# Performance work log

Hardware: AMD Instinct MI355X
Metric: run time of the kernel (lower is better)

Reference implementation:

```python
import jax, jax.numpy as jnp
import numpy as np

B, S, DIM, H, DH = 2, 2048, 1024, 16, 64
EPS = 1e-6


def rms_norm(x, w):
    # x: (..., DH); computed in fp32 like the torch module
    norm = jax.lax.rsqrt(jnp.mean(jnp.square(x), axis=-1, keepdims=True) + EPS)
    return (x * norm) * w


def apply_rope(x, freqs):
    # x: (B, H, S, D), freqs: (S, D); torch code slices cos/sin to first half
    d = x.shape[-1] // 2
    cos = jnp.cos(freqs)[None, None, :, :d]
    sin = jnp.sin(freqs)[None, None, :, :d]
    x1, x2 = x[..., :d], x[..., d:]
    return jnp.concatenate([x1 * cos - x2 * sin, x2 * cos + x1 * sin], axis=-1)


def setup_inputs() -> dict:
    key = jax.random.key(0)
    ks = jax.random.split(key, 4)
    x = jax.random.normal(ks[0], (B, S, DIM), dtype=jnp.float32)
    # causal additive mask
    causal = jnp.tril(jnp.ones((S, S), dtype=bool))
    mask = jnp.where(causal, 0.0, -1e9).astype(jnp.float32)[None, None]
    # standard rope frequencies: pos * inv_freq over head_dim
    inv_freq = 1.0 / (10000.0 ** (jnp.arange(0, DH, dtype=jnp.float32) / DH))
    rope_freqs = jnp.arange(S, dtype=jnp.float32)[:, None] * inv_freq[None, :]
    total = H * DH
    w_qkv = jax.random.normal(ks[1], (3 * total, DIM), dtype=jnp.float32) * (DIM ** -0.5)
    w_out = jax.random.normal(ks[2], (DIM, total), dtype=jnp.float32) * (total ** -0.5)
    q_norm_w = jnp.ones((DH,), dtype=jnp.float32)
    k_norm_w = jnp.ones((DH,), dtype=jnp.float32)
    return {"x": x, "mask": mask, "rope_freqs": rope_freqs, "w_qkv": w_qkv,
            "w_out": w_out, "q_norm_w": q_norm_w, "k_norm_w": k_norm_w}


def reference(x, mask, rope_freqs, w_qkv, w_out, q_norm_w, k_norm_w):
    b, s, _ = x.shape
    qkv = (x @ w_qkv.T).reshape(b, s, 3, H, DH)
    q, k, v = qkv[:, :, 0], qkv[:, :, 1], qkv[:, :, 2]
    q = jnp.transpose(rms_norm(q, q_norm_w), (0, 2, 1, 3))  # (B,H,S,DH)
    k = jnp.transpose(rms_norm(k, k_norm_w), (0, 2, 1, 3))
    v = jnp.transpose(v, (0, 2, 1, 3))
    q = apply_rope(q, rope_freqs)
    k = apply_rope(k, rope_freqs)
    scale = DH ** -0.5
    attn = jnp.einsum('bhsd,bhtd->bhst', q, k) * scale + mask
    attn = jax.nn.softmax(attn, axis=-1)
    out = jnp.einsum('bhst,bhtd->bhsd', attn, v)
    out = jnp.transpose(out, (0, 2, 1, 3)).reshape(b, s, H * DH)
    return out @ w_out.T
```

## Files before the change

kernel.cpp:

```cpp
#include <hip/hip_runtime.h>
#include <hip/hip_bf16.h>
#include <stdint.h>

typedef short bf16x8 __attribute__((ext_vector_type(8)));
typedef float f32x4  __attribute__((ext_vector_type(4)));

#define MFMA_BF16(a,b,c) __builtin_amdgcn_mfma_f32_16x16x32_bf16((a),(b),(c),0,0,0)

__device__ __forceinline__ void async_ld16(const void* g, void* l) {
  __builtin_amdgcn_global_load_lds(
      (const __attribute__((address_space(1))) void*)g,
      (__attribute__((address_space(3))) void*)l, 16, 0, 0);
}

__device__ __forceinline__ unsigned short bf16_bits(float x) {
  __hip_bfloat16 h = __float2bfloat16(x);
  return *(unsigned short*)&h;
}

#define NX_C    (2 * 2048 * 1024)
#define NWQKV_C (3072 * 1024)
#define NWOUT_C (1024 * 1024)

__global__ void __launch_bounds__(256)
cvt_all(const float* __restrict__ x, const float* __restrict__ wqkv,
        const float* __restrict__ wout, __hip_bfloat16* __restrict__ dst)
{
  const int i = (blockIdx.x * 256 + threadIdx.x) * 4;
  const float* src;
  int off;
  if (i < NX_C)                { src = x;    off = i; }
  else if (i < NX_C + NWQKV_C) { src = wqkv; off = i - NX_C; }
  else                         { src = wout; off = i - NX_C - NWQKV_C; }
  const float4 v = *(const float4*)(src + off);
  ushort4 u;
  u.x = bf16_bits(v.x); u.y = bf16_bits(v.y);
  u.z = bf16_bits(v.z); u.w = bf16_bits(v.w);
  *(ushort4*)((unsigned short*)dst + i) = u;
}

template<int EPI>
__global__ void __launch_bounds__(256)
gemm_bt(const __hip_bfloat16* __restrict__ A,
        const __hip_bfloat16* __restrict__ B,
        int K,
        __hip_bfloat16* __restrict__ o0,
        __hip_bfloat16* __restrict__ o1,
        __hip_bfloat16* __restrict__ o2,
        float* __restrict__ of,
        const float* __restrict__ freqs,
        const float* __restrict__ qw,
        const float* __restrict__ kw)
{
  __shared__ __align__(16) __hip_bfloat16 As[2][128 * 32];
  __shared__ __align__(16) __hip_bfloat16 Bs[2][64 * 32];

  const int tid  = threadIdx.x;
  const int w    = tid >> 6;
  const int lane = tid & 63;
  const int quad = lane >> 4;
  const int l15  = lane & 15;

  const int m0 = blockIdx.y * 128;
  const int n0 = blockIdx.x * 64;

  const int srow = lane >> 2;
  const int sgr  = ((lane & 3) ^ ((lane >> 3) & 3)) * 8;
  const int c0 = w * 2, c1 = w * 2 + 1;

  const int pg = l15 * 32 + (quad ^ ((l15 >> 1) & 3)) * 8;

  const int wm  = w * 32;
  const int ac0 = w * 2;

  f32x4 acc[2][4] = {};

#define GSTAGE(KN, BUF) do {                                                        \
    async_ld16(A + (size_t)(m0 + c0 * 16 + srow) * K + (KN) + sgr,                  \
               &As[BUF][0] + c0 * 512);                                             \
    async_ld16(A + (size_t)(m0 + c1 * 16 + srow) * K + (KN) + sgr,                  \
               &As[BUF][0] + c1 * 512);                                             \
    async_ld16(B + (size_t)(n0 + w * 16 + srow) * K + (KN) + sgr,                   \
               &Bs[BUF][0] + w * 512);                                              \
  } while (0)

  const int niter = K >> 5;
  GSTAGE(0, 0);

  for (int it = 0; it < niter; ++it) {
    const int cur = it & 1;
    __syncthreads();
    if (it + 1 < niter) GSTAGE((it + 1) << 5, cur ^ 1);

    const __hip_bfloat16* Ac = &As[cur][0];
    const __hip_bfloat16* Bc = &Bs[cur][0];
    bf16x8 af[2], bfr[4];
    af[0] = *(const bf16x8*)(Ac + (ac0 + 0) * 512 + pg);
    af[1] = *(const bf16x8*)(Ac + (ac0 + 1) * 512 + pg);
#pragma unroll
    for (int t = 0; t < 4; ++t)
      bfr[t] = *(const bf16x8*)(Bc + t * 512 + pg);
#pragma unroll
    for (int mt = 0; mt < 2; ++mt)
#pragma unroll
      for (int nt = 0; nt < 4; ++nt)
        acc[mt][nt] = MFMA_BF16(af[mt], bfr[nt], acc[mt][nt]);
  }
#undef GSTAGE

  if (EPI == 1) {
    const int ldc = (int)gridDim.x * 64;
#pragma unroll
    for (int mt = 0; mt < 2; ++mt)
#pragma unroll
      for (int nt = 0; nt < 4; ++nt)
#pragma unroll
        for (int r = 0; r < 4; ++r)
          of[(size_t)(m0 + wm + mt * 16 + quad * 4 + r) * ldc
             + n0 + nt * 16 + l15] = acc[mt][nt][r];
    return;
  }

  const int which = n0 >> 10;
  const int hb    = (n0 & 1023) >> 6;

  if (which == 2) {
#pragma unroll
    for (int mt = 0; mt < 2; ++mt)
#pragma unroll
      for (int nt = 0; nt < 4; ++nt)
#pragma unroll
        for (int r = 0; r < 4; ++r) {
          const int m = m0 + wm + mt * 16 + quad * 4 + r;
          const int b = m >> 11, s = m & 2047;
          const int d = nt * 16 + l15;
          o2[((size_t)((b * 16 + hb) * 64 + d) << 11) + s] =
              __float2bfloat16(acc[mt][nt][r]);
        }
    return;
  }

  const float* wgt = which ? kw : qw;
  __hip_bfloat16* dst = which ? o1 : o0;
  const float wv0 = wgt[l15], wv1 = wgt[16 + l15];
  const float wv2 = wgt[32 + l15], wv3 = wgt[48 + l15];

#pragma unroll
  for (int mt = 0; mt < 2; ++mt) {
#pragma unroll
    for (int r = 0; r < 4; ++r) {
      float ssq = acc[mt][0][r] * acc[mt][0][r] + acc[mt][1][r] * acc[mt][1][r]
                + acc[mt][2][r] * acc[mt][2][r] + acc[mt][3][r] * acc[mt][3][r];
      ssq += __shfl_xor(ssq, 1);
      ssq += __shfl_xor(ssq, 2);
      ssq += __shfl_xor(ssq, 4);
      ssq += __shfl_xor(ssq, 8);
      float sc = rsqrtf(ssq * (1.0f / 64.0f) + 1e-6f);
      if (which == 0) sc *= 0.125f;

      const float y0 = acc[mt][0][r] * sc * wv0;
      const float y1 = acc[mt][1][r] * sc * wv1;
      const float y2 = acc[mt][2][r] * sc * wv2;
      const float y3 = acc[mt][3][r] * sc * wv3;

      const int m = m0 + wm + mt * 16 + quad * 4 + r;
      const int b = m >> 11, s = m & 2047;
      const float f0 = freqs[s * 64 + l15];
      const float f1 = freqs[s * 64 + 16 + l15];
      float sn0, cs0, sn1, cs1;
      __sincosf(f0, &sn0, &cs0);
      __sincosf(f1, &sn1, &cs1);

      const size_t row = ((size_t)((b * 16 + hb) * 2048 + s)) << 6;
      dst[row + l15]      = __float2bfloat16(y0 * cs0 - y2 * sn0);
      dst[row + 16 + l15] = __float2bfloat16(y1 * cs1 - y3 * sn1);
      dst[row + 32 + l15] = __float2bfloat16(y2 * cs0 + y0 * sn0);
      dst[row + 48 + l15] = __float2bfloat16(y3 * cs1 + y1 * sn1);
    }
  }
}

__global__ void __launch_bounds__(256, 2)
attn(const __hip_bfloat16* __restrict__ q,
     const __hip_bfloat16* __restrict__ k,
     const __hip_bfloat16* __restrict__ vt,
     __hip_bfloat16* __restrict__ ao)
{
  __shared__ __align__(16) __hip_bfloat16 Ks[2][64 * 64];
  __shared__ __align__(16) __hip_bfloat16 Vs[2][64 * 64];

  const int tid  = threadIdx.x;
  const int w    = tid >> 6;
  const int lane = tid & 63;
  const int quad = lane >> 4;
  const int l15  = lane & 15;

  const int lin  = blockIdx.x;
  const int c8   = lin & 7;
  const int rest = lin >> 3;
  const int pj   = rest & 15;
  const int bh   = ((rest >> 4) << 3) + c8;
  const int b    = bh >> 4, h = bh & 15;

  const __hip_bfloat16* qb = q  + (size_t)bh * 2048 * 64;
  const __hip_bfloat16* kb = k  + (size_t)bh * 2048 * 64;
  const __hip_bfloat16* vb = vt + (size_t)bh * 64 * 2048;

  const int pr = ((l15 >> 2) * 8) + (l15 & 3);

  const int pgk  = (quad ^ (l15 & 3) ^ (((l15 >> 2) & 1) << 2)) * 8;
  const int pgk4 = pgk ^ 32;
  const int pgv  = (quad ^ (l15 & 7)) * 8;
  const int pgv4 = pgv ^ 32;

  const int sj  = lane >> 3;
  const int sp  = lane & 7;
  const int kgA = (sp ^ (sj & 3)) * 8;
  const int kgB = kgA ^ 32;
  const int vgs = (sp ^ sj) * 8;
  const int ck0 = w * 2, ck1 = w * 2 + 1;

#define STAGE(KEY0, BUF) do {                                                     \
    __hip_bfloat16* ks_ = &Ks[BUF][0];                                            \
    __hip_bfloat16* vs_ = &Vs[BUF][0];                                            \
    async_ld16(kb + (size_t)((KEY0) + ck0 * 8 + sj) * 64 + kgA, ks_ + ck0 * 512); \
    async_ld16(kb + (size_t)((KEY0) + ck1 * 8 + sj) * 64 + kgB, ks_ + ck1 * 512); \
    async_ld16(vb + (size_t)(ck0 * 8 + sj) * 2048 + (KEY0) + vgs, vs_ + ck0 * 512); \
    async_ld16(vb + (size_t)(ck1 * 8 + sj) * 2048 + (KEY0) + vgs, vs_ + ck1 * 512); \
  } while (0)

  for (int pass = 0; pass < 2; ++pass) {
    const int J  = pass ? (31 - pj) : pj;
    const int q0 = J * 64 + w * 16;
    const int qi = q0 + l15;

    const bf16x8 bq0 = *(const bf16x8*)(qb + (size_t)qi * 64 + quad * 8);
    const bf16x8 bq1 = *(const bf16x8*)(qb + (size_t)qi * 64 + 32 + quad * 8);

    f32x4 o[4] = {};
    float lsum = 0.f;

    const int ntile = J + 1;

    __syncthreads();
    STAGE(0, 0);

    for (int kt = 0; kt < ntile; ++kt) {
      const int cur = kt & 1;
      const int t0 = kt * 64;

      __syncthreads();
      if (kt + 1 < ntile) STAGE(t0 + 64, cur ^ 1);

      const __hip_bfloat16* Kc = &Ks[cur][0];
      const __hip_bfloat16* Vc = &Vs[cur][0];

      bf16x8 ka00, ka01, ka10, ka11, kb00, kb01, kb10, kb11;
      ka00 = *(const bf16x8*)(Kc + (pr)      * 64 + pgk);
      ka01 = *(const bf16x8*)(Kc + (pr)      * 64 + pgk4);
      ka10 = *(const bf16x8*)(Kc + (pr + 4)  * 64 + pgk);
      ka11 = *(const bf16x8*)(Kc + (pr + 4)  * 64 + pgk4);
      kb00 = *(const bf16x8*)(Kc + (32 + pr)     * 64 + pgk);
      kb01 = *(const bf16x8*)(Kc + (32 + pr)     * 64 + pgk4);
      kb10 = *(const bf16x8*)(Kc + (32 + pr + 4) * 64 + pgk);
      kb11 = *(const bf16x8*)(Kc + (32 + pr + 4) * 64 + pgk4);

      bf16x8 va[2][4];
#pragma unroll
      for (int dt = 0; dt < 4; ++dt) {
        va[0][dt] = *(const bf16x8*)(Vc + (dt * 16 + l15) * 64 + pgv);
        va[1][dt] = *(const bf16x8*)(Vc + (dt * 16 + l15) * 64 + pgv4);
      }

      f32x4 c00 = {}, c01 = {}, c10 = {}, c11 = {};
      c00 = MFMA_BF16(ka00, bq0, c00); c00 = MFMA_BF16(ka01, bq1, c00);
      c01 = MFMA_BF16(ka10, bq0, c01); c01 = MFMA_BF16(ka11, bq1, c01);
      c10 = MFMA_BF16(kb00, bq0, c10); c10 = MFMA_BF16(kb01, bq1, c10);
      c11 = MFMA_BF16(kb10, bq0, c11); c11 = MFMA_BF16(kb11, bq1, c11);

      float e00[4], e01[4], e10[4], e11[4];
#pragma unroll
      for (int r = 0; r < 4; ++r) {
        e00[r] = c00[r]; e01[r] = c01[r]; e10[r] = c10[r]; e11[r] = c11[r];
      }

      if (kt == ntile - 1) {
#pragma unroll
        for (int r = 0; r < 4; ++r) {
          const int k0v = t0 + 8 * quad + r;
          if (k0v      > qi) e00[r] = -1e30f;
          if (k0v + 4  > qi) e01[r] = -1e30f;
          if (k0v + 32 > qi) e10[r] = -1e30f;
          if (k0v + 36 > qi) e11[r] = -1e30f;
        }
      }

      float rs = 0.f;
#pragma unroll
      for (int r = 0; r < 4; ++r) {
        e00[r] = __expf(e00[r] - 8.0f);
        e01[r] = __expf(e01[r] - 8.0f);
        e10[r] = __expf(e10[r] - 8.0f);
        e11[r] = __expf(e11[r] - 8.0f);
        rs += (e00[r] + e01[r]) + (e10[r] + e11[r]);
      }
      lsum += rs;

      bf16x8 pf0, pf1;
#pragma unroll
      for (int r = 0; r < 4; ++r) {
        pf0[r] = (short)bf16_bits(e00[r]);  pf0[r + 4] = (short)bf16_bits(e01[r]);
        pf1[r] = (short)bf16_bits(e10[r]);  pf1[r + 4] = (short)bf16_bits(e11[r]);
      }

#pragma unroll
      for (int dt = 0; dt < 4; ++dt) {
        o[dt] = MFMA_BF16(va[0][dt], pf0, o[dt]);
        o[dt] = MFMA_BF16(va[1][dt], pf1, o[dt]);
      }
    }

    lsum += __shfl_xor(lsum, 16);
    lsum += __shfl_xor(lsum, 32);

    const float inv = 1.0f / lsum;
    const size_t row = ((size_t)(b * 2048 + qi)) * 1024 + h * 64;
#pragma unroll
    for (int dt = 0; dt < 4; ++dt) {
      ushort4 u;
      u.x = bf16_bits(o[dt][0] * inv);
      u.y = bf16_bits(o[dt][1] * inv);
      u.z = bf16_bits(o[dt][2] * inv);
      u.w = bf16_bits(o[dt][3] * inv);
      *(ushort4*)((unsigned short*)ao + row + dt * 16 + quad * 4) = u;
    }
  }
#undef STAGE
}

extern "C" void kernel_launch(void* const* d_in, const int* in_sizes, int n_in,
                              void* d_out, int out_size, void* d_ws, size_t ws_size,
                              hipStream_t stream)
{
  const float* x    = (const float*)d_in[0];
  const float* rf   = (const float*)d_in[2];
  const float* wqkv = (const float*)d_in[3];
  const float* wout = (const float*)d_in[4];
  const float* qw   = (const float*)d_in[5];
  const float* kw   = (const float*)d_in[6];

  const size_t NE = (size_t)2 * 16 * 2048 * 64;

  __hip_bfloat16* qb  = (__hip_bfloat16*)d_ws;
  __hip_bfloat16* kb  = qb  + NE;
  __hip_bfloat16* vt  = kb  + NE;
  __hip_bfloat16* ao  = vt  + NE;
  __hip_bfloat16* xb  = ao  + NE;
  __hip_bfloat16* wqb = xb  + NX_C;
  __hip_bfloat16* wob = wqb + NWQKV_C;

  cvt_all<<<(NX_C + NWQKV_C + NWOUT_C) / 1024, 256, 0, stream>>>(x, wqkv, wout, xb);

  gemm_bt<0><<<dim3(48, 32), 256, 0, stream>>>(xb, wqb, 1024, qb, kb, vt,
                                               nullptr, rf, qw, kw);
  attn<<<512, 256, 0, stream>>>(qb, kb, vt, ao);
  gemm_bt<1><<<dim3(16, 32), 256, 0, stream>>>(ao, wob, 1024,
                                               nullptr, nullptr, nullptr, (float*)d_out,
                                               nullptr, nullptr, nullptr);
}
```

Measured before the change: 200.1 us.

## Enlarge GEMM tiles to 256x256 with 8 waves and interleaved async pipeline

The bf16 GEMM is rewritten to use 256x256 output tiles per 512-thread block, with each wave owning a 128x64 sub-tile. The K loop now advances 64 at a time, splits each step into sub-phases, and issues the next stage's async global-to-LDS loads between MFMA bursts. It uses explicit waitcnt, barriers and setprio to overlap loads with compute. The larger tiles raise operand reuse and cut global traffic, but they shrink the grid to fewer blocks than CUs, especially for the output projection, and they raise register and LDS pressure.

```diff
diff --git a/kernel.cpp b/kernel.cpp
--- a/kernel.cpp
+++ b/kernel.cpp
@@ -40,7 +40,7 @@
 }
 
 template<int EPI>
-__global__ void __launch_bounds__(256)
+__global__ void __launch_bounds__(512)
 gemm_bt(const __hip_bfloat16* __restrict__ A,
         const __hip_bfloat16* __restrict__ B,
         int K,
@@ -52,8 +52,8 @@
         const float* __restrict__ qw,
         const float* __restrict__ kw)
 {
-  __shared__ __align__(16) __hip_bfloat16 As[2][128 * 32];
-  __shared__ __align__(16) __hip_bfloat16 Bs[2][64 * 32];
+  __shared__ __align__(16) __hip_bfloat16 As[2][2][16 * 512];
+  __shared__ __align__(16) __hip_bfloat16 Bs[2][2][16 * 512];
 
   const int tid  = threadIdx.x;
   const int w    = tid >> 6;
@@ -61,77 +61,154 @@
   const int quad = lane >> 4;
   const int l15  = lane & 15;
 
-  const int m0 = blockIdx.y * 128;
-  const int n0 = blockIdx.x * 64;
+  const int m0 = blockIdx.y * 256;
+  const int n0 = blockIdx.x * 256;
 
   const int srow = lane >> 2;
   const int sgr  = ((lane & 3) ^ ((lane >> 3) & 3)) * 8;
-  const int c0 = w * 2, c1 = w * 2 + 1;
 
   const int pg = l15 * 32 + (quad ^ ((l15 >> 1) & 3)) * 8;
 
-  const int wm  = w * 32;
-  const int ac0 = w * 2;
-
-  f32x4 acc[2][4] = {};
-
-#define GSTAGE(KN, BUF) do {                                                        \
-    async_ld16(A + (size_t)(m0 + c0 * 16 + srow) * K + (KN) + sgr,                  \
-               &As[BUF][0] + c0 * 512);                                             \
-    async_ld16(A + (size_t)(m0 + c1 * 16 + srow) * K + (KN) + sgr,                  \
-               &As[BUF][0] + c1 * 512);                                             \
-    async_ld16(B + (size_t)(n0 + w * 16 + srow) * K + (KN) + sgr,                   \
-               &Bs[BUF][0] + w * 512);                                              \
+  const int wmh   = w >> 2;
+  const int wnq   = w & 3;
+  const int abase = wmh * 8;
+  const int bbase = wnq * 4;
+
+  f32x4 acc[8][4] = {};
+
+#define SGROUP(KSX, KSUB, NB) do {                                                   \
+    const int kn_ = (KSX) * 64 + (KSUB) * 32 + sgr;                                  \
+    async_ld16(A + (size_t)(m0 + (2 * w + 0) * 16 + srow) * K + kn_,                 \
+               &As[NB][KSUB][(2 * w + 0) * 512]);                                    \
+    async_ld16(A + (size_t)(m0 + (2 * w + 1) * 16 + srow) * K + kn_,                 \
+               &As[NB][KSUB][(2 * w + 1) * 512]);                                    \
+    async_ld16(B + (size_t)(n0 + (2 * w + 0) * 16 + srow) * K + kn_,                 \
+               &Bs[NB][KSUB][(2 * w + 0) * 512]);                                    \
+    async_ld16(B + (size_t)(n0 + (2 * w + 1) * 16 + srow) * K + kn_,                 \
+               &Bs[NB][KSUB][(2 * w + 1) * 512]);                                    \
   } while (0)
 
-  const int niter = K >> 5;
-  GSTAGE(0, 0);
-
-  for (int it = 0; it < niter; ++it) {
-    const int cur = it & 1;
-    __syncthreads();
-    if (it + 1 < niter) GSTAGE((it + 1) << 5, cur ^ 1);
-
-    const __hip_bfloat16* Ac = &As[cur][0];
-    const __hip_bfloat16* Bc = &Bs[cur][0];
-    bf16x8 af[2], bfr[4];
-    af[0] = *(const bf16x8*)(Ac + (ac0 + 0) * 512 + pg);
-    af[1] = *(const bf16x8*)(Ac + (ac0 + 1) * 512 + pg);
-#pragma unroll
-    for (int t = 0; t < 4; ++t)
-      bfr[t] = *(const bf16x8*)(Bc + t * 512 + pg);
-#pragma unroll
-    for (int mt = 0; mt < 2; ++mt)
+#define MFMA16(MB, a0, a1, a2, a3) do {                                              \
+    __builtin_amdgcn_s_setprio(1);                                                   \
+    acc[(MB)+0][0] = MFMA_BF16(a0, bf0, acc[(MB)+0][0]);                             \
+    acc[(MB)+0][1] = MFMA_BF16(a0, bf1, acc[(MB)+0][1]);                             \
+    acc[(MB)+0][2] = MFMA_BF16(a0, bf2, acc[(MB)+0][2]);                             \
+    acc[(MB)+0][3] = MFMA_BF16(a0, bf3, acc[(MB)+0][3]);                             \
+    acc[(MB)+1][0] = MFMA_BF16(a1, bf0, acc[(MB)+1][0]);                             \
+    acc[(MB)+1][1] = MFMA_BF16(a1, bf1, acc[(MB)+1][1]);                             \
+    acc[(MB)+1][2] = MFMA_BF16(a1, bf2, acc[(MB)+1][2]);                             \
+    acc[(MB)+1][3] = MFMA_BF16(a1, bf3, acc[(MB)+1][3]);                             \
+    acc[(MB)+2][0] = MFMA_BF16(a2, bf0, acc[(MB)+2][0]);                             \
+    acc[(MB)+2][1] = MFMA_BF16(a2, bf1, acc[(MB)+2][1]);                             \
+    acc[(MB)+2][2] = MFMA_BF16(a2, bf2, acc[(MB)+2][2]);                             \
+    acc[(MB)+2][3] = MFMA_BF16(a2, bf3, acc[(MB)+2][3]);                             \
+    acc[(MB)+3][0] = MFMA_BF16(a3, bf0, acc[(MB)+3][0]);                             \
+    acc[(MB)+3][1] = MFMA_BF16(a3, bf1, acc[(MB)+3][1]);                             \
+    acc[(MB)+3][2] = MFMA_BF16(a3, bf2, acc[(MB)+3][2]);                             \
+    acc[(MB)+3][3] = MFMA_BF16(a3, bf3, acc[(MB)+3][3]);                             \
+    __builtin_amdgcn_s_setprio(0);                                                   \
+  } while (0)
+
+  const int nks = K >> 6;
+
+  SGROUP(0, 0, 0);
+  SGROUP(0, 1, 0);
+  asm volatile("s_waitcnt vmcnt(4)" ::: "memory");
+  __builtin_amdgcn_s_barrier();
+
+  for (int ks = 0; ks < nks; ++ks) {
+    const int cur = ks & 1;
+    const int nb  = cur ^ 1;
+    const bool stg = (ks + 1 < nks);
+    bf16x8 bf0, bf1, bf2, bf3;
+
+    {
+      const __hip_bfloat16* Ac = &As[cur][0][0];
+      const __hip_bfloat16* Bc = &Bs[cur][0][0];
+      bf16x8 a0 = *(const bf16x8*)(Ac + (abase + 0) * 512 + pg);
+      bf16x8 a1 = *(const bf16x8*)(Ac + (abase + 1) * 512 + pg);
+      bf16x8 a2 = *(const bf16x8*)(Ac + (abase + 2) * 512 + pg);
+      bf16x8 a3 = *(const bf16x8*)(Ac + (abase + 3) * 512 + pg);
+      bf0 = *(const bf16x8*)(Bc + (bbase + 0) * 512 + pg);
+      bf1 = *(const bf16x8*)(Bc + (bbase + 1) * 512 + pg);
+      bf2 = *(const bf16x8*)(Bc + (bbase + 2) * 512 + pg);
+      bf3 = *(const bf16x8*)(Bc + (bbase + 3) * 512 + pg);
+      if (stg) SGROUP(ks + 1, 0, nb);
+      __builtin_amdgcn_s_barrier();
+      asm volatile("s_waitcnt lgkmcnt(0)" ::: "memory");
+      MFMA16(0, a0, a1, a2, a3);
+      __builtin_amdgcn_s_barrier();
+    }
+    {
+      const __hip_bfloat16* Ac = &As[cur][0][0];
+      bf16x8 a0 = *(const bf16x8*)(Ac + (abase + 4) * 512 + pg);
+      bf16x8 a1 = *(const bf16x8*)(Ac + (abase + 5) * 512 + pg);
+      bf16x8 a2 = *(const bf16x8*)(Ac + (abase + 6) * 512 + pg);
+      bf16x8 a3 = *(const bf16x8*)(Ac + (abase + 7) * 512 + pg);
+      if (stg) SGROUP(ks + 1, 1, nb);
+      __builtin_amdgcn_s_barrier();
+      asm volatile("s_waitcnt lgkmcnt(0)" ::: "memory");
+      MFMA16(4, a0, a1, a2, a3);
+      if (stg) asm volatile("s_waitcnt vmcnt(4)" ::: "memory");
+      else     asm volatile("s_waitcnt vmcnt(0)" ::: "memory");
+      __builtin_amdgcn_s_barrier();
+    }
+    {
+      const __hip_bfloat16* Ac = &As[cur][1][0];
+      const __hip_bfloat16* Bc = &Bs[cur][1][0];
+      bf16x8 a0 = *(const bf16x8*)(Ac + (abase + 0) * 512 + pg);
+      bf16x8 a1 = *(const bf16x8*)(Ac + (abase + 1) * 512 + pg);
+      bf16x8 a2 = *(const bf16x8*)(Ac + (abase + 2) * 512 + pg);
+      bf16x8 a3 = *(const bf16x8*)(Ac + (abase + 3) * 512 + pg);
+      bf0 = *(const bf16x8*)(Bc + (bbase + 0) * 512 + pg);
+      bf1 = *(const bf16x8*)(Bc + (bbase + 1) * 512 + pg);
+      bf2 = *(const bf16x8*)(Bc + (bbase + 2) * 512 + pg);
+      bf3 = *(const bf16x8*)(Bc + (bbase + 3) * 512 + pg);
+      __builtin_amdgcn_s_barrier();
+      asm volatile("s_waitcnt lgkmcnt(0)" ::: "memory");
+      MFMA16(0, a0, a1, a2, a3);
+      __builtin_amdgcn_s_barrier();
+    }
+    {
+      const __hip_bfloat16* Ac = &As[cur][1][0];
+      bf16x8 a0 = *(const bf16x8*)(Ac + (abase + 4) * 512 + pg);
+      bf16x8 a1 = *(const bf16x8*)(Ac + (abase + 5) * 512 + pg);
+      bf16x8 a2 = *(const bf16x8*)(Ac + (abase + 6) * 512 + pg);
+      bf16x8 a3 = *(const bf16x8*)(Ac + (abase + 7) * 512 + pg);
+      __builtin_amdgcn_s_barrier();
+      asm volatile("s_waitcnt lgkmcnt(0)" ::: "memory");
+      MFMA16(4, a0, a1, a2, a3);
+      if (stg) asm volatile("s_waitcnt vmcnt(4)" ::: "memory");
+      __builtin_amdgcn_s_barrier();
+    }
+  }
+#undef SGROUP
+#undef MFMA16
+
+  if (EPI == 1) {
+    const int ldc = (int)gridDim.x * 256;
+#pragma unroll
+    for (int mt = 0; mt < 8; ++mt)
 #pragma unroll
       for (int nt = 0; nt < 4; ++nt)
-        acc[mt][nt] = MFMA_BF16(af[mt], bfr[nt], acc[mt][nt]);
-  }
-#undef GSTAGE
-
-  if (EPI == 1) {
-    const int ldc = (int)gridDim.x * 64;
-#pragma unroll
-    for (int mt = 0; mt < 2; ++mt)
-#pragma unroll
-      for (int nt = 0; nt < 4; ++nt)
 #pragma unroll
         for (int r = 0; r < 4; ++r)
-          of[(size_t)(m0 + wm + mt * 16 + quad * 4 + r) * ldc
-             + n0 + nt * 16 + l15] = acc[mt][nt][r];
+          of[(size_t)(m0 + wmh * 128 + mt * 16 + quad * 4 + r) * ldc
+             + n0 + wnq * 64 + nt * 16 + l15] = acc[mt][nt][r];
     return;
   }
 
   const int which = n0 >> 10;
-  const int hb    = (n0 & 1023) >> 6;
+  const int hb    = ((n0 & 1023) >> 6) + wnq;
 
   if (which == 2) {
 #pragma unroll
-    for (int mt = 0; mt < 2; ++mt)
+    for (int mt = 0; mt < 8; ++mt)
 #pragma unroll
       for (int nt = 0; nt < 4; ++nt)
 #pragma unroll
         for (int r = 0; r < 4; ++r) {
-          const int m = m0 + wm + mt * 16 + quad * 4 + r;
+          const int m = m0 + wmh * 128 + mt * 16 + quad * 4 + r;
           const int b = m >> 11, s = m & 2047;
           const int d = nt * 16 + l15;
           o2[((size_t)((b * 16 + hb) * 64 + d) << 11) + s] =
@@ -146,7 +223,7 @@
   const float wv2 = wgt[32 + l15], wv3 = wgt[48 + l15];
 
 #pragma unroll
-  for (int mt = 0; mt < 2; ++mt) {
+  for (int mt = 0; mt < 8; ++mt) {
 #pragma unroll
     for (int r = 0; r < 4; ++r) {
       float ssq = acc[mt][0][r] * acc[mt][0][r] + acc[mt][1][r] * acc[mt][1][r]
@@ -163,7 +240,7 @@
       const float y2 = acc[mt][2][r] * sc * wv2;
       const float y3 = acc[mt][3][r] * sc * wv3;
 
-      const int m = m0 + wm + mt * 16 + quad * 4 + r;
+      const int m = m0 + wmh * 128 + mt * 16 + quad * 4 + r;
       const int b = m >> 11, s = m & 2047;
       const float f0 = freqs[s * 64 + l15];
       const float f1 = freqs[s * 64 + 16 + l15];
@@ -361,10 +438,10 @@
 
   cvt_all<<<(NX_C + NWQKV_C + NWOUT_C) / 1024, 256, 0, stream>>>(x, wqkv, wout, xb);
 
-  gemm_bt<0><<<dim3(48, 32), 256, 0, stream>>>(xb, wqb, 1024, qb, kb, vt,
+  gemm_bt<0><<<dim3(12, 16), 512, 0, stream>>>(xb, wqb, 1024, qb, kb, vt,
                                                nullptr, rf, qw, kw);
   attn<<<512, 256, 0, stream>>>(qb, kb, vt, ao);
-  gemm_bt<1><<<dim3(16, 32), 256, 0, stream>>>(ao, wob, 1024,
-                                               nullptr, nullptr, nullptr, (float*)d_out,
-                                               nullptr, nullptr, nullptr);
-}
+  gemm_bt<1><<<dim3(4, 16), 512, 0, stream>>>(ao, wob, 1024,
+                                              nullptr, nullptr, nullptr, (float*)d_out,
+                                              nullptr, nullptr, nullptr);
+}
```

Measured after the change: 211.3 us. 1.06x slower.
